# Optimization experiments

Measured on AMD Instinct MI355X. Metric: run time of the kernel, lower is better.

Reference implementation:

```python
import jax, jax.numpy as jnp
import numpy as np

B, L, K, I, O = 4, 10000, 16, 256, 256


def setup_inputs() -> dict:
    key = jax.random.key(0)
    k1, k2, k3 = jax.random.split(key, 3)
    x = jax.random.normal(k1, (B, L, I), dtype=jnp.float32)
    index_tensor = jax.random.randint(k2, (L, K), 0, L, dtype=jnp.int64)
    stdv = 0.5
    mask = jax.random.uniform(k3, (K, I, O), dtype=jnp.float32, minval=-stdv, maxval=stdv)
    bias = jnp.zeros((O,), dtype=jnp.float32)
    return {"x": x, "index_tensor": index_tensor, "mask": mask, "bias": bias}


def reference(x, index_tensor, mask, bias):
    # torch: expand x to [b,l,l,i], gather along dim2 with index[l,k] -> [b,l,k,i]
    # equivalent: per output node n, neighbors x[:, index_tensor[n, j], :]
    gathered = x[:, index_tensor, :]            # [b, l, k, i]
    # flatten(k,i) @ flatten(mask: [k*i, o]) == einsum over k,i
    y = jnp.einsum('blki,kio->blo', gathered, mask) + bias
    return y
```

## Files before the change

### kernel.cpp

```cpp
#include <hip/hip_runtime.h>

#define Bdim 4
#define Ldim 10000
#define Kdim 16
#define Idim 256
#define Odim 256

typedef __attribute__((ext_vector_type(8))) __bf16 bf16x8;
typedef __attribute__((ext_vector_type(4))) float f32x4;

__global__ __launch_bounds__(256)
void prepack(const float* __restrict__ x, const float* __restrict__ mask,
             __bf16* __restrict__ xb, __bf16* __restrict__ wpk)
{
    const int b = blockIdx.x;
    if (b < 2500) {
        const size_t base = ((size_t)b * 256 + threadIdx.x) * 16;
#pragma unroll
        for (int j = 0; j < 2; ++j) {
            const float4 f0 = *(const float4*)(x + base + j * 8);
            const float4 f1 = *(const float4*)(x + base + j * 8 + 4);
            bf16x8 v;
            v[0] = (__bf16)f0.x; v[1] = (__bf16)f0.y; v[2] = (__bf16)f0.z; v[3] = (__bf16)f0.w;
            v[4] = (__bf16)f1.x; v[5] = (__bf16)f1.y; v[6] = (__bf16)f1.z; v[7] = (__bf16)f1.w;
            *(bf16x8*)(xb + base + j * 8) = v;
        }
    } else {
        const int tg = (b - 2500) * 256 + threadIdx.x;
        const int c  = tg >> 6;
        const int ln = tg & 63;
        const int ni  = c & 3;
        const int ks  = (c >> 2) & 1;
        const int wid = (c >> 3) & 3;
        const int kb  = c >> 5;
        const int n   = wid * 64 + ni * 16 + (ln & 15);
        const int kk0 = kb * 64 + ks * 32 + (ln >> 4) * 8;
        bf16x8 v;
#pragma unroll
        for (int j = 0; j < 8; ++j)
            v[j] = (__bf16)mask[(size_t)(kk0 + j) * Odim + n];
        *(bf16x8*)(wpk + (size_t)tg * 8) = v;
    }
}

#define TL 20
#define BM 80
#define IDXS 17

#define BARRIER() do { asm volatile("s_waitcnt lgkmcnt(0)" ::: "memory"); \
                       __builtin_amdgcn_s_barrier(); } while (0)

__global__ __launch_bounds__(256, 2)
void piconv_gemm(const __bf16* __restrict__ xb,
                 const int* __restrict__ idxT,
                 const __bf16* __restrict__ wpk,
                 const float* __restrict__ bias,
                 float* __restrict__ out)
{
    __shared__ __bf16 Alds[2][BM * 64];
    __shared__ int    idx_lds[TL * IDXS];

    const int t    = threadIdx.x;
    const int l0   = blockIdx.x * TL;
    const int lane = t & 63;
    const int wid  = t >> 6;
    const int q    = lane >> 4;
    const int r16  = lane & 15;

    {
        const int e0 = t;
        idx_lds[(e0 >> 4) * IDXS + (e0 & 15)] = idxT[l0 * Kdim + e0];
        if (t < 64) {
            const int e1 = t + 256;
            idx_lds[(e1 >> 4) * IDXS + (e1 & 15)] = idxT[l0 * Kdim + e1];
        }
    }

    const int rA = t & 31,               pA = t >> 5;
    const int rB = 32 + (t & 31);
    const int rC = 64 + ((t >> 1) & 15);
    const bool cAct = (t & 1) == 0;
    const int abbA = rA / TL, altA = rA % TL;
    const int abbB = rB / TL, altB = rB % TL;
    const int abbC = rC / TL, altC = rC % TL;
    const size_t abaseA = ((size_t)abbA * Ldim) << 8;
    const size_t abaseB = ((size_t)abbB * Ldim) << 8;
    const size_t abaseC = ((size_t)abbC * Ldim) << 8;
    const int dsA = (((rA >> 4) * 2 + (pA >> 2)) * 512) + ((pA & 3) * 128) + ((rA & 15) * 8);
    const int dsB = (((rB >> 4) * 2 + (pA >> 2)) * 512) + ((pA & 3) * 128) + ((rB & 15) * 8);
    const int dsC = (((rC >> 4) * 2 + (pA >> 2)) * 512) + ((pA & 3) * 128) + ((rC & 15) * 8);
    const int po  = pA * 8;

    const __bf16* wbase = wpk + ((size_t)(wid * 8) << 9) + lane * 8;

    f32x4  acc[5][4] = {};
    bf16x8 aRA, aRB, aRC;
    bf16x8 wA[8], wB[8];

    __syncthreads();

    {
        const int ivA = idx_lds[altA * IDXS];
        const int ivB = idx_lds[altB * IDXS];
        aRA = *(const bf16x8*)(xb + abaseA + (((size_t)ivA) << 8) + po);
        aRB = *(const bf16x8*)(xb + abaseB + (((size_t)ivB) << 8) + po);
        if (cAct) {
            const int ivC = idx_lds[altC * IDXS];
            aRC = *(const bf16x8*)(xb + abaseC + (((size_t)ivC) << 8) + po);
        }
#pragma unroll
        for (int j = 0; j < 8; ++j)
            wA[j] = *(const bf16x8*)(wbase + j * 512);
    }

#define STEP(S, WCUR, WNXT, PFA, PFW)                                           \
    {                                                                           \
        __bf16* db = &Alds[(S) & 1][0];                                         \
        *(bf16x8*)(db + dsA) = aRA;                                             \
        *(bf16x8*)(db + dsB) = aRB;                                             \
        if (cAct) *(bf16x8*)(db + dsC) = aRC;                                   \
        BARRIER();                                                              \
        if (PFA) {                                           \
            const int T   = (S) + 1;                                            \
            const int kn  = T >> 2;                                             \
            const int iob = ((T & 3) << 6) + po;                                \
            const int ivA = idx_lds[altA * IDXS + kn];                          \
            const int ivB = idx_lds[altB * IDXS + kn];                          \
            aRA = *(const bf16x8*)(xb + abaseA + (((size_t)ivA) << 8) + iob);   \
            aRB = *(const bf16x8*)(xb + abaseB + (((size_t)ivB) << 8) + iob);   \
            if (cAct) {                                                         \
                const int ivC = idx_lds[altC * IDXS + kn];                      \
                aRC = *(const bf16x8*)(xb + abaseC + (((size_t)ivC) << 8) + iob); \
            }                                                                   \
        }                                                                       \
        if (PFW) {                                                  \
            const __bf16* wq = wbase + ((size_t)((S) + 1)) * 16384;             \
            _Pragma("unroll")                                                   \
            for (int j = 0; j < 8; ++j)                                         \
                WNXT[j] = *(const bf16x8*)(wq + j * 512);                       \
        }                                                                       \
        _Pragma("unroll")                                                       \
        for (int ks = 0; ks < 2; ++ks) {                                        \
            bf16x8 af[5];                                                       \
            _Pragma("unroll")                                                   \
            for (int mi = 0; mi < 5; ++mi)                                      \
                af[mi] = *(const bf16x8*)(&Alds[(S) & 1][(mi * 2 + ks) * 512 + lane * 8]); \
            _Pragma("unroll")                                                   \
            for (int mi = 0; mi < 5; ++mi)                                      \
                _Pragma("unroll")                                               \
                for (int ni = 0; ni < 4; ++ni)                                  \
                    acc[mi][ni] = __builtin_amdgcn_mfma_f32_16x16x32_bf16(      \
                        af[mi], WCUR[ks * 4 + ni], acc[mi][ni], 0, 0, 0);       \
        }                                                                       \
    }

    for (int s2 = 0; s2 < 31; ++s2) {
        STEP(2 * s2,     wA, wB, true, true)
        STEP(2 * s2 + 1, wB, wA, true, true)
    }
    STEP(62, wA, wB, true,  true)
    STEP(63, wB, wA, false, false)
#undef STEP

    float bv[4];
#pragma unroll
    for (int ni = 0; ni < 4; ++ni)
        bv[ni] = bias[wid * 64 + ni * 16 + r16];
#pragma unroll
    for (int mi = 0; mi < 5; ++mi) {
#pragma unroll
        for (int rr = 0; rr < 4; ++rr) {
            const int r  = mi * 16 + q * 4 + rr;
            const int ab = r / TL;
            const int al = r % TL;
            float* dst = out + (((size_t)(ab * Ldim + l0 + al)) << 8) + wid * 64 + r16;
#pragma unroll
            for (int ni = 0; ni < 4; ++ni)
                dst[ni * 16] = acc[mi][ni][rr] + bv[ni];
        }
    }
}

#define FTL 32
#define FBN 128
#define FLDA 72
__global__ __launch_bounds__(256)
void piconv_fallback(const float* __restrict__ x,
                     const int* __restrict__ idxT,
                     const float* __restrict__ mask,
                     const float* __restrict__ bias,
                     float* __restrict__ out)
{
    __shared__ __bf16 Alds[128 * FLDA];
    __shared__ __bf16 Wlds[FBN * FLDA];
    const int t  = threadIdx.x;
    const int l0 = blockIdx.x * FTL;
    const int n0 = blockIdx.y * FBN;
    const int lane = t & 63;
    const int wid  = t >> 6;
    const int wm   = wid >> 1;
    const int wn   = wid & 1;
    const int q    = lane >> 4;
    const int r16  = lane & 15;
    f32x4 acc[4][4] = {};
    const int am    = t >> 1;
    const int ahalf = t & 1;
    const int alt   = am & 31;
    const int abb   = am >> 5;
    const int al    = l0 + alt;
    const bool avalid = (al < Ldim);
    for (int kb = 0; kb < 64; ++kb) {
        {
            const int ksl = kb >> 2;
            const int i0  = ((kb & 3) << 6) + (ahalf << 5);
            const int idx = avalid ? idxT[al * Kdim + ksl] : 0;
            const float* src = x + (((size_t)(abb * Ldim + idx)) << 8) + i0;
#pragma unroll
            for (int j = 0; j < 4; ++j) {
                const float4 f0 = *(const float4*)(src + j * 8);
                const float4 f1 = *(const float4*)(src + j * 8 + 4);
                bf16x8 v;
                v[0] = (__bf16)f0.x; v[1] = (__bf16)f0.y; v[2] = (__bf16)f0.z; v[3] = (__bf16)f0.w;
                v[4] = (__bf16)f1.x; v[5] = (__bf16)f1.y; v[6] = (__bf16)f1.z; v[7] = (__bf16)f1.w;
                *(bf16x8*)&Alds[am * FLDA + (ahalf << 5) + j * 8] = v;
            }
        }
        {
#pragma unroll
            for (int it = 0; it < 4; ++it) {
                const int pair = t + it * 256;
                const int n    = pair & 127;
                const int g    = pair >> 7;
                const float* src = mask + (((size_t)(kb * 64 + g * 8)) << 8) + n0 + n;
                bf16x8 v;
#pragma unroll
                for (int j = 0; j < 8; ++j)
                    v[j] = (__bf16)src[(size_t)j << 8];
                *(bf16x8*)&Wlds[n * FLDA + g * 8] = v;
            }
        }
        __syncthreads();
#pragma unroll
        for (int ks = 0; ks < 2; ++ks) {
            bf16x8 af[4], bfr[4];
#pragma unroll
            for (int mi = 0; mi < 4; ++mi)
                af[mi] = *(bf16x8*)&Alds[(wm * 64 + mi * 16 + r16) * FLDA + ks * 32 + q * 8];
#pragma unroll
            for (int ni = 0; ni < 4; ++ni)
                bfr[ni] = *(bf16x8*)&Wlds[(wn * 64 + ni * 16 + r16) * FLDA + ks * 32 + q * 8];
#pragma unroll
            for (int mi = 0; mi < 4; ++mi)
#pragma unroll
                for (int ni = 0; ni < 4; ++ni)
                    acc[mi][ni] = __builtin_amdgcn_mfma_f32_16x16x32_bf16(
                        af[mi], bfr[ni], acc[mi][ni], 0, 0, 0);
        }
        __syncthreads();
    }
    float bv[4];
#pragma unroll
    for (int ni = 0; ni < 4; ++ni)
        bv[ni] = bias[n0 + wn * 64 + ni * 16 + r16];
#pragma unroll
    for (int mi = 0; mi < 4; ++mi) {
        const int mrow = wm * 64 + mi * 16 + q * 4;
#pragma unroll
        for (int rr = 0; rr < 4; ++rr) {
            const int m  = mrow + rr;
            const int lt = m & 31;
            const int bb = m >> 5;
            const int l  = l0 + lt;
            if (l < Ldim) {
                float* dst = out + (((size_t)(bb * Ldim + l)) << 8) + n0 + wn * 64 + r16;
#pragma unroll
                for (int ni = 0; ni < 4; ++ni)
                    dst[ni * 16] = acc[mi][ni][rr] + bv[ni];
            }
        }
    }
}

extern "C" void kernel_launch(void* const* d_in, const int* in_sizes, int n_in,
                              void* d_out, int out_size, void* d_ws, size_t ws_size,
                              hipStream_t stream) {
    const float* x    = (const float*)d_in[0];
    const int*   idx  = (const int*)d_in[1];
    const float* mask = (const float*)d_in[2];
    const float* bias = (const float*)d_in[3];
    float* out = (float*)d_out;

    const size_t xb_bytes = (size_t)Bdim * Ldim * Idim * 2;
    const size_t wp_bytes = (size_t)Kdim * Idim * Odim * 2;

    if (ws_size >= xb_bytes + wp_bytes) {
        __bf16* xb  = (__bf16*)d_ws;
        __bf16* wpk = (__bf16*)((char*)d_ws + xb_bytes);
        prepack<<<2500 + 512, 256, 0, stream>>>(x, mask, xb, wpk);
        piconv_gemm<<<Ldim / TL, 256, 0, stream>>>(xb, idx, wpk, bias, out);
    } else {
        dim3 grid((Ldim + FTL - 1) / FTL, Odim / FBN, 1);
        piconv_fallback<<<grid, 256, 0, stream>>>(x, idx, mask, bias, out);
    }
}
```

Baseline: 178.8 us.

## Double K-chunk per stage to halve barriers and restructure gather staging

Each pipeline stage now stages 128 input channels instead of 64, which doubles the LDS A buffer and halves the number of barrier-separated steps (32 instead of 64). Every thread now issues five gathered 16-byte loads per stage with unified index math, replacing the earlier uneven A/B/C split. Weight prefetch is interleaved inside the stage so the next two weight chunks load during the MFMAs. This cuts synchronization overhead and gives memory latency more time to hide, at the cost of more LDS and more live registers, which could hurt occupancy.

```diff
diff --git a/kernel.cpp b/kernel.cpp
--- a/kernel.cpp
+++ b/kernel.cpp
@@ -57,7 +57,7 @@
                  const float* __restrict__ bias,
                  float* __restrict__ out)
 {
-    __shared__ __bf16 Alds[2][BM * 64];
+    __shared__ __bf16 Alds[2][BM * 128];
     __shared__ int    idx_lds[TL * IDXS];
 
     const int t    = threadIdx.x;
@@ -76,91 +76,129 @@
         }
     }
 
-    const int rA = t & 31,               pA = t >> 5;
-    const int rB = 32 + (t & 31);
-    const int rC = 64 + ((t >> 1) & 15);
-    const bool cAct = (t & 1) == 0;
-    const int abbA = rA / TL, altA = rA % TL;
-    const int abbB = rB / TL, altB = rB % TL;
-    const int abbC = rC / TL, altC = rC % TL;
-    const size_t abaseA = ((size_t)abbA * Ldim) << 8;
-    const size_t abaseB = ((size_t)abbB * Ldim) << 8;
-    const size_t abaseC = ((size_t)abbC * Ldim) << 8;
-    const int dsA = (((rA >> 4) * 2 + (pA >> 2)) * 512) + ((pA & 3) * 128) + ((rA & 15) * 8);
-    const int dsB = (((rB >> 4) * 2 + (pA >> 2)) * 512) + ((pA & 3) * 128) + ((rB & 15) * 8);
-    const int dsC = (((rC >> 4) * 2 + (pA >> 2)) * 512) + ((pA & 3) * 128) + ((rC & 15) * 8);
-    const int po  = pA * 8;
+    int    alt_[5], dsb_[5], go_[5];
+    size_t abase_[5];
+#pragma unroll
+    for (int j = 0; j < 5; ++j) {
+        const int u = t + j * 256;
+        const int r = u % 80;
+        const int p = u / 80;
+        alt_[j]   = r % TL;
+        abase_[j] = ((size_t)(r / TL) * Ldim) << 8;
+        dsb_[j]   = ((r >> 4) * 4 + (p >> 2)) * 1024 + (p & 3) * 256 + (r & 15) * 16;
+        go_[j]    = p * 8;
+    }
 
     const __bf16* wbase = wpk + ((size_t)(wid * 8) << 9) + lane * 8;
 
     f32x4  acc[5][4] = {};
-    bf16x8 aRA, aRB, aRC;
+    bf16x8 aR[5];
     bf16x8 wA[8], wB[8];
 
     __syncthreads();
 
+#pragma unroll
+    for (int j = 0; j < 5; ++j) {
+        const int iv = idx_lds[alt_[j] * IDXS];
+        aR[j] = *(const bf16x8*)(xb + abase_[j] + (((size_t)iv) << 8) + go_[j]);
+    }
+#pragma unroll
+    for (int j = 0; j < 8; ++j)
+        wA[j] = *(const bf16x8*)(wbase + j * 512);
+
+    for (int S = 0; S < 31; ++S) {
+        char* db = (char*)&Alds[S & 1][0];
+#pragma unroll
+        for (int j = 0; j < 5; ++j)
+            *(bf16x8*)(db + dsb_[j]) = aR[j];
+        BARRIER();
+        {
+            const int kn  = (S + 1) >> 1;
+            const int iob = ((S + 1) & 1) << 7;
+#pragma unroll
+            for (int j = 0; j < 5; ++j) {
+                const int iv = idx_lds[alt_[j] * IDXS + kn];
+                aR[j] = *(const bf16x8*)(xb + abase_[j] + (((size_t)iv) << 8) + iob + go_[j]);
+            }
+        }
+        {
+            const __bf16* wq = wbase + ((size_t)(2 * S + 1)) * 16384;
+#pragma unroll
+            for (int j = 0; j < 8; ++j)
+                wB[j] = *(const bf16x8*)(wq + j * 512);
+        }
+#pragma unroll
+        for (int ks = 0; ks < 2; ++ks) {
+            bf16x8 af[5];
+#pragma unroll
+            for (int mi = 0; mi < 5; ++mi)
+                af[mi] = *(const bf16x8*)(db + (mi * 4 + ks) * 1024 + lane * 16);
+#pragma unroll
+            for (int mi = 0; mi < 5; ++mi)
+#pragma unroll
+                for (int ni = 0; ni < 4; ++ni)
+                    acc[mi][ni] = __builtin_amdgcn_mfma_f32_16x16x32_bf16(
+                        af[mi], wA[ks * 4 + ni], acc[mi][ni], 0, 0, 0);
+        }
+        {
+            const __bf16* wq = wbase + ((size_t)(2 * S + 2)) * 16384;
+#pragma unroll
+            for (int j = 0; j < 8; ++j)
+                wA[j] = *(const bf16x8*)(wq + j * 512);
+        }
+#pragma unroll
+        for (int ks = 2; ks < 4; ++ks) {
+            bf16x8 af[5];
+#pragma unroll
+            for (int mi = 0; mi < 5; ++mi)
+                af[mi] = *(const bf16x8*)(db + (mi * 4 + ks) * 1024 + lane * 16);
+#pragma unroll
+            for (int mi = 0; mi < 5; ++mi)
+#pragma unroll
+                for (int ni = 0; ni < 4; ++ni)
+                    acc[mi][ni] = __builtin_amdgcn_mfma_f32_16x16x32_bf16(
+                        af[mi], wB[(ks - 2) * 4 + ni], acc[mi][ni], 0, 0, 0);
+        }
+    }
     {
-        const int ivA = idx_lds[altA * IDXS];
-        const int ivB = idx_lds[altB * IDXS];
-        aRA = *(const bf16x8*)(xb + abaseA + (((size_t)ivA) << 8) + po);
-        aRB = *(const bf16x8*)(xb + abaseB + (((size_t)ivB) << 8) + po);
-        if (cAct) {
-            const int ivC = idx_lds[altC * IDXS];
-            aRC = *(const bf16x8*)(xb + abaseC + (((size_t)ivC) << 8) + po);
-        }
-#pragma unroll
-        for (int j = 0; j < 8; ++j)
-            wA[j] = *(const bf16x8*)(wbase + j * 512);
-    }
-
-#define STEP(S, WCUR, WNXT, PFA, PFW)                                           \
-    {                                                                           \
-        __bf16* db = &Alds[(S) & 1][0];                                         \
-        *(bf16x8*)(db + dsA) = aRA;                                             \
-        *(bf16x8*)(db + dsB) = aRB;                                             \
-        if (cAct) *(bf16x8*)(db + dsC) = aRC;                                   \
-        BARRIER();                                                              \
-        if (PFA) {                                           \
-            const int T   = (S) + 1;                                            \
-            const int kn  = T >> 2;                                             \
-            const int iob = ((T & 3) << 6) + po;                                \
-            const int ivA = idx_lds[altA * IDXS + kn];                          \
-            const int ivB = idx_lds[altB * IDXS + kn];                          \
-            aRA = *(const bf16x8*)(xb + abaseA + (((size_t)ivA) << 8) + iob);   \
-            aRB = *(const bf16x8*)(xb + abaseB + (((size_t)ivB) << 8) + iob);   \
-            if (cAct) {                                                         \
-                const int ivC = idx_lds[altC * IDXS + kn];                      \
-                aRC = *(const bf16x8*)(xb + abaseC + (((size_t)ivC) << 8) + iob); \
-            }                                                                   \
-        }                                                                       \
-        if (PFW) {                                                  \
-            const __bf16* wq = wbase + ((size_t)((S) + 1)) * 16384;             \
-            _Pragma("unroll")                                                   \
-            for (int j = 0; j < 8; ++j)                                         \
-                WNXT[j] = *(const bf16x8*)(wq + j * 512);                       \
-        }                                                                       \
-        _Pragma("unroll")                                                       \
-        for (int ks = 0; ks < 2; ++ks) {                                        \
-            bf16x8 af[5];                                                       \
-            _Pragma("unroll")                                                   \
-            for (int mi = 0; mi < 5; ++mi)                                      \
-                af[mi] = *(const bf16x8*)(&Alds[(S) & 1][(mi * 2 + ks) * 512 + lane * 8]); \
-            _Pragma("unroll")                                                   \
-            for (int mi = 0; mi < 5; ++mi)                                      \
-                _Pragma("unroll")                                               \
-                for (int ni = 0; ni < 4; ++ni)                                  \
-                    acc[mi][ni] = __builtin_amdgcn_mfma_f32_16x16x32_bf16(      \
-                        af[mi], WCUR[ks * 4 + ni], acc[mi][ni], 0, 0, 0);       \
-        }                                                                       \
-    }
-
-    for (int s2 = 0; s2 < 31; ++s2) {
-        STEP(2 * s2,     wA, wB, true, true)
-        STEP(2 * s2 + 1, wB, wA, true, true)
-    }
-    STEP(62, wA, wB, true,  true)
-    STEP(63, wB, wA, false, false)
-#undef STEP
+        char* db = (char*)&Alds[1][0];
+#pragma unroll
+        for (int j = 0; j < 5; ++j)
+            *(bf16x8*)(db + dsb_[j]) = aR[j];
+        BARRIER();
+        {
+            const __bf16* wq = wbase + ((size_t)63) * 16384;
+#pragma unroll
+            for (int j = 0; j < 8; ++j)
+                wB[j] = *(const bf16x8*)(wq + j * 512);
+        }
+#pragma unroll
+        for (int ks = 0; ks < 2; ++ks) {
+            bf16x8 af[5];
+#pragma unroll
+            for (int mi = 0; mi < 5; ++mi)
+                af[mi] = *(const bf16x8*)(db + (mi * 4 + ks) * 1024 + lane * 16);
+#pragma unroll
+            for (int mi = 0; mi < 5; ++mi)
+#pragma unroll
+                for (int ni = 0; ni < 4; ++ni)
+                    acc[mi][ni] = __builtin_amdgcn_mfma_f32_16x16x32_bf16(
+                        af[mi], wA[ks * 4 + ni], acc[mi][ni], 0, 0, 0);
+        }
+#pragma unroll
+        for (int ks = 2; ks < 4; ++ks) {
+            bf16x8 af[5];
+#pragma unroll
+            for (int mi = 0; mi < 5; ++mi)
+                af[mi] = *(const bf16x8*)(db + (mi * 4 + ks) * 1024 + lane * 16);
+#pragma unroll
+            for (int mi = 0; mi < 5; ++mi)
+#pragma unroll
+                for (int ni = 0; ni < 4; ++ni)
+                    acc[mi][ni] = __builtin_amdgcn_mfma_f32_16x16x32_bf16(
+                        af[mi], wB[(ks - 2) * 4 + ni], acc[mi][ni], 0, 0, 0);
+        }
+    }
 
     float bv[4];
 #pragma unroll
```

New measurement: 197.8 us. 1.11x slower.

## Remap gather thread mapping, XOR-swizzle LDS tile, raise MFMA wave priority

Applied to the files above, without the earlier changes.

Reassigns which thread gathers which row/column chunk so that four consecutive threads read one contiguous 64-byte segment of a neighbor row, and the third load is handled by whole waves (t<128) instead of alternate lanes. The LDS A-tile gets a new byte layout with an XOR swizzle to cut bank conflicts on both stores and fragment reads. The MFMA section is wrapped in s_setprio to favor waves issuing matrix work. The added index arithmetic and changed layout could introduce mapping errors or extra address ALU work.

```diff
diff --git a/kernel.cpp b/kernel.cpp
--- a/kernel.cpp
+++ b/kernel.cpp
@@ -76,37 +76,39 @@
         }
     }
 
-    const int rA = t & 31,               pA = t >> 5;
-    const int rB = 32 + (t & 31);
-    const int rC = 64 + ((t >> 1) & 15);
-    const bool cAct = (t & 1) == 0;
-    const int abbA = rA / TL, altA = rA % TL;
-    const int abbB = rB / TL, altB = rB % TL;
-    const int abbC = rC / TL, altC = rC % TL;
-    const size_t abaseA = ((size_t)abbA * Ldim) << 8;
-    const size_t abaseB = ((size_t)abbB * Ldim) << 8;
-    const size_t abaseC = ((size_t)abbC * Ldim) << 8;
-    const int dsA = (((rA >> 4) * 2 + (pA >> 2)) * 512) + ((pA & 3) * 128) + ((rA & 15) * 8);
-    const int dsB = (((rB >> 4) * 2 + (pA >> 2)) * 512) + ((pA & 3) * 128) + ((rB & 15) * 8);
-    const int dsC = (((rC >> 4) * 2 + (pA >> 2)) * 512) + ((pA & 3) * 128) + ((rC & 15) * 8);
-    const int po  = pA * 8;
+    const int p4 = t & 3;
+    int    alt_[3], dsb_[3], goff_[3];
+    size_t abase_[3];
+#pragma unroll
+    for (int j = 0; j < 3; ++j) {
+        const int u = (t >> 2) + 64 * j;
+        const int r = u % 80;
+        const int h = u / 80;
+        alt_[j]   = r % TL;
+        abase_[j] = ((size_t)(r / TL) * Ldim) << 8;
+        dsb_[j]   = ((r >> 4) * 2 + h) * 1024
+                  + ((p4 * 256 + (r & 15) * 16) ^ (p4 << 5));
+        goff_[j]  = h * 32 + p4 * 8;
+    }
+    const bool j2 = (t < 128);
+    const int aoff = ((lane >> 4) * 256 + r16 * 16) ^ ((lane >> 4) << 5);
 
     const __bf16* wbase = wpk + ((size_t)(wid * 8) << 9) + lane * 8;
 
     f32x4  acc[5][4] = {};
-    bf16x8 aRA, aRB, aRC;
+    bf16x8 aR[3];
     bf16x8 wA[8], wB[8];
 
     __syncthreads();
 
     {
-        const int ivA = idx_lds[altA * IDXS];
-        const int ivB = idx_lds[altB * IDXS];
-        aRA = *(const bf16x8*)(xb + abaseA + (((size_t)ivA) << 8) + po);
-        aRB = *(const bf16x8*)(xb + abaseB + (((size_t)ivB) << 8) + po);
-        if (cAct) {
-            const int ivC = idx_lds[altC * IDXS];
-            aRC = *(const bf16x8*)(xb + abaseC + (((size_t)ivC) << 8) + po);
+        const int iv0 = idx_lds[alt_[0] * IDXS];
+        const int iv1 = idx_lds[alt_[1] * IDXS];
+        aR[0] = *(const bf16x8*)(xb + abase_[0] + (((size_t)iv0) << 8) + goff_[0]);
+        aR[1] = *(const bf16x8*)(xb + abase_[1] + (((size_t)iv1) << 8) + goff_[1]);
+        if (j2) {
+            const int iv2 = idx_lds[alt_[2] * IDXS];
+            aR[2] = *(const bf16x8*)(xb + abase_[2] + (((size_t)iv2) << 8) + goff_[2]);
         }
 #pragma unroll
         for (int j = 0; j < 8; ++j)
@@ -115,22 +117,22 @@
 
 #define STEP(S, WCUR, WNXT, PFA, PFW)                                           \
     {                                                                           \
-        __bf16* db = &Alds[(S) & 1][0];                                         \
-        *(bf16x8*)(db + dsA) = aRA;                                             \
-        *(bf16x8*)(db + dsB) = aRB;                                             \
-        if (cAct) *(bf16x8*)(db + dsC) = aRC;                                   \
+        char* db = (char*)&Alds[(S) & 1][0];                                    \
+        *(bf16x8*)(db + dsb_[0]) = aR[0];                                       \
+        *(bf16x8*)(db + dsb_[1]) = aR[1];                                       \
+        if (j2) *(bf16x8*)(db + dsb_[2]) = aR[2];                               \
         BARRIER();                                                              \
         if (PFA) {                                           \
             const int T   = (S) + 1;                                            \
             const int kn  = T >> 2;                                             \
-            const int iob = ((T & 3) << 6) + po;                                \
-            const int ivA = idx_lds[altA * IDXS + kn];                          \
-            const int ivB = idx_lds[altB * IDXS + kn];                          \
-            aRA = *(const bf16x8*)(xb + abaseA + (((size_t)ivA) << 8) + iob);   \
-            aRB = *(const bf16x8*)(xb + abaseB + (((size_t)ivB) << 8) + iob);   \
-            if (cAct) {                                                         \
-                const int ivC = idx_lds[altC * IDXS + kn];                      \
-                aRC = *(const bf16x8*)(xb + abaseC + (((size_t)ivC) << 8) + iob); \
+            const int iob = (T & 3) << 6;                                       \
+            const int iv0 = idx_lds[alt_[0] * IDXS + kn];                       \
+            const int iv1 = idx_lds[alt_[1] * IDXS + kn];                       \
+            aR[0] = *(const bf16x8*)(xb + abase_[0] + (((size_t)iv0) << 8) + iob + goff_[0]); \
+            aR[1] = *(const bf16x8*)(xb + abase_[1] + (((size_t)iv1) << 8) + iob + goff_[1]); \
+            if (j2) {                                                           \
+                const int iv2 = idx_lds[alt_[2] * IDXS + kn];                   \
+                aR[2] = *(const bf16x8*)(xb + abase_[2] + (((size_t)iv2) << 8) + iob + goff_[2]); \
             }                                                                   \
         }                                                                       \
         if (PFW) {                                                  \
@@ -139,12 +141,13 @@
             for (int j = 0; j < 8; ++j)                                         \
                 WNXT[j] = *(const bf16x8*)(wq + j * 512);                       \
         }                                                                       \
+        __builtin_amdgcn_s_setprio(1);                                          \
         _Pragma("unroll")                                                       \
         for (int ks = 0; ks < 2; ++ks) {                                        \
             bf16x8 af[5];                                                       \
             _Pragma("unroll")                                                   \
             for (int mi = 0; mi < 5; ++mi)                                      \
-                af[mi] = *(const bf16x8*)(&Alds[(S) & 1][(mi * 2 + ks) * 512 + lane * 8]); \
+                af[mi] = *(const bf16x8*)(db + (mi * 2 + ks) * 1024 + aoff);    \
             _Pragma("unroll")                                                   \
             for (int mi = 0; mi < 5; ++mi)                                      \
                 _Pragma("unroll")                                               \
@@ -152,6 +155,7 @@
                     acc[mi][ni] = __builtin_amdgcn_mfma_f32_16x16x32_bf16(      \
                         af[mi], WCUR[ks * 4 + ni], acc[mi][ni], 0, 0, 0);       \
         }                                                                       \
+        __builtin_amdgcn_s_setprio(0);                                          \
     }
 
     for (int s2 = 0; s2 < 31; ++s2) {
```

Result: no change. 180.8 us (+1.1%).
